# Kernel optimization log

Hardware: AMD Instinct MI355X
Metric: run time of the kernel (lower is better)

The kernel has to match this reference:

```python
import jax, jax.numpy as jnp
import numpy as np

B, H, W, C = 16, 112, 112, 128
WS, SS, NH = 7, 3, 4  # window_size, shift_size, num_heads
EPS = 1e-5


def _ln(x, g, b):
    m = jnp.mean(x, axis=-1, keepdims=True)
    v = jnp.var(x, axis=-1, keepdims=True)
    return (x - m) * jax.lax.rsqrt(v + EPS) * g + b


def _rel_index(w):
    # standard Swin relative-position index, [w*w, w*w] int
    coords = np.stack(np.meshgrid(np.arange(w), np.arange(w), indexing='ij'))  # [2,w,w]
    flat = coords.reshape(2, -1)                      # [2, N]
    rel = (flat[:, :, None] - flat[:, None, :]).transpose(1, 2, 0)  # [N,N,2]
    rel = rel + (w - 1)
    return rel[..., 0] * (2 * w - 1) + rel[..., 1]


def _attn_mask(Hp, Wp, w, s):
    # standard Swin shifted-window attention mask, [nW, N, N] float32 (0 / -100)
    img = np.zeros((Hp, Wp))
    cnt = 0
    for hs in (slice(0, -w), slice(-w, -s), slice(-s, None)):
        for ws_ in (slice(0, -w), slice(-w, -s), slice(-s, None)):
            img[hs, ws_] = cnt
            cnt += 1
    mw = img.reshape(Hp // w, w, Wp // w, w).transpose(0, 2, 1, 3).reshape(-1, w * w)
    d = mw[:, None, :] - mw[:, :, None]
    return np.where(d != 0, -100.0, 0.0).astype(np.float32)


def setup_inputs() -> dict:
    key = jax.random.key(0)
    ks = jax.random.split(key, 8)
    f = lambda k, shape: jax.random.normal(k, shape, dtype=jnp.float32) * 0.02
    return dict(
        x=jax.random.normal(ks[0], (B, H, W, C), dtype=jnp.float32),
        norm1_g=jnp.ones((C,), jnp.float32), norm1_b=jnp.zeros((C,), jnp.float32),
        qkv_w=f(ks[1], (C, 3 * C)), qkv_b=jnp.zeros((3 * C,), jnp.float32),
        rel_table=f(ks[2], ((2 * WS - 1) ** 2, NH)),
        proj_w=f(ks[3], (C, C)), proj_b=jnp.zeros((C,), jnp.float32),
        norm2_g=jnp.ones((C,), jnp.float32), norm2_b=jnp.zeros((C,), jnp.float32),
        fc1_w=f(ks[4], (C, 4 * C)), fc1_b=jnp.zeros((4 * C,), jnp.float32),
        fc2_w=f(ks[5], (4 * C, C)), fc2_b=jnp.zeros((C,), jnp.float32),
    )


def reference(x, norm1_g, norm1_b, qkv_w, qkv_b, rel_table, proj_w, proj_b,
              norm2_g, norm2_b, fc1_w, fc1_b, fc2_w, fc2_b):
    w, s, nH = WS, SS, NH
    hd = C // nH
    N = w * w
    scale = hd ** -0.5

    shortcut = x
    xn = _ln(x, norm1_g, norm1_b)
    # cyclic shift (H, W already multiples of w -> no padding)
    xs = jnp.roll(xn, (-s, -s), axis=(1, 2)) if s > 0 else xn
    # window partition -> [B*nW, N, C]
    wins = xs.reshape(B, H // w, w, W // w, w, C).transpose(0, 1, 3, 2, 4, 5).reshape(-1, N, C)

    qkv = wins @ qkv_w + qkv_b  # [M, N, 3C]
    q, k, v = [t.reshape(-1, N, nH, hd).transpose(0, 2, 1, 3)
               for t in jnp.split(qkv, 3, axis=-1)]
    attn = jnp.einsum('mhqd,mhkd->mhqk', q * scale, k)  # [M, nH, N, N]

    idx = _rel_index(w)  # static numpy [N, N]
    bias = rel_table[idx.reshape(-1)].reshape(N, N, nH).transpose(2, 0, 1)  # [nH, N, N]
    attn = attn + bias[None]

    if s > 0:
        mask = jnp.asarray(_attn_mask(H, W, w, s))  # [nW, N, N] static
        nW = mask.shape[0]
        attn = (attn.reshape(B, nW, nH, N, N) + mask[None, :, None]).reshape(-1, nH, N, N)

    attn = jax.nn.softmax(attn, axis=-1)
    out = jnp.einsum('mhqk,mhkd->mhqd', attn, v).transpose(0, 2, 1, 3).reshape(-1, N, C)
    out = out @ proj_w + proj_b

    # window reverse + unshift
    x_attn = out.reshape(B, H // w, W // w, w, w, C).transpose(0, 1, 3, 2, 4, 5).reshape(B, H, W, C)
    if s > 0:
        x_attn = jnp.roll(x_attn, (s, s), axis=(1, 2))

    x1 = shortcut + x_attn
    xn2 = _ln(x1, norm2_g, norm2_b)
    hdd = jax.nn.gelu(xn2 @ fc1_w + fc1_b, approximate=False)  # torch nn.GELU (exact)
    return x1 + (hdd @ fc2_w + fc2_b)
```

## Files before the change

kernel.cpp:

```cpp
#include <hip/hip_runtime.h>
#include <stdint.h>

typedef unsigned short u16;
typedef unsigned int   u32;
typedef __attribute__((ext_vector_type(8))) short bh8;
typedef __attribute__((ext_vector_type(4))) float f32x4;

#define SCALE 0.17677669529663687f
#define MFMA  __builtin_amdgcn_mfma_f32_16x16x32_bf16

#define WS_QKV  0
#define WS_PROJ 49152
#define WS_F1   65536
#define WS_F2   131072
#define WS_M    196608
#define WS_QB   327680

__device__ __forceinline__ u16 f2bf(float f){
    u32 i; __builtin_memcpy(&i,&f,4); i += 0x7fffu + ((i>>16)&1u); return (u16)(i>>16);
}
__device__ __forceinline__ u32 cvtpk(float lo, float hi){
    u32 r; asm("v_cvt_pk_bf16_f32 %0, %1, %2" : "=v"(r) : "v"(lo), "v"(hi)); return r;
}
__device__ __forceinline__ float rcpf(float v){
    float r; asm("v_rcp_f32 %0, %1" : "=v"(r) : "v"(v)); return r;
}
union BH8U { bh8 v; u32 u[4]; };

__global__ void prep_k(const float* __restrict__ qkvw, const float* __restrict__ projw,
                       const float* __restrict__ f1w,  const float* __restrict__ f2w,
                       const float* __restrict__ rel,  const float* __restrict__ qkvb,
                       u16* __restrict__ ws)
{
    int idx = blockIdx.x * 256 + threadIdx.x;
    if (idx < 49152) {
        int c = idx / 384, j = idx % 384;
        float v = qkvw[idx] * (j < 128 ? SCALE : 1.0f);
        ws[WS_QKV + j * 128 + c] = f2bf(v);
    } else if (idx < 65536) {
        int i = idx - 49152; int k = i >> 7, j = i & 127;
        int pk = (k & ~31) | ((k & 15) << 1) | ((k >> 4) & 1);
        ws[WS_PROJ + j * 128 + pk] = f2bf(projw[i]);
    } else if (idx < 131072) {
        int i = idx - 65536; int c = i >> 9, j = i & 511;
        ws[WS_F1 + j * 128 + c] = f2bf(f1w[i]);
    } else if (idx < 196608) {
        int i = idx - 131072; int k = i >> 7, j = i & 127;
        int pk = (k & ~31) | ((k & 15) << 1) | ((k >> 4) & 1);
        ws[WS_F2 + j * 512 + pk] = f2bf(f2w[i]);
    } else if (idx < 262144) {
        int m = idx - 196608;
        int jr = m & 3, lane = (m >> 2) & 63, tct = (m >> 8) & 15;
        int h = (m >> 12) & 3, cls = (m >> 14) & 3;
        int rt = tct >> 2, ct = tct & 3;
        int row = rt * 16 + (lane >> 4) * 4 + jr, key = ct * 16 + (lane & 15);
        float v;
        if (row < 49 && key < 49) {
            int ri = row / 7, rc = row % 7, ki = key / 7, kc = key % 7;
            v = rel[((ri - ki + 6) * 13 + (rc - kc + 6)) * 4 + h];
            int rH = (cls & 2) ? (ri < 4 ? 1 : 2) : 0, rW = (cls & 1) ? (rc < 4 ? 1 : 2) : 0;
            int kH = (cls & 2) ? (ki < 4 ? 1 : 2) : 0, kW = (cls & 1) ? (kc < 4 ? 1 : 2) : 0;
            if (rH * 3 + rW != kH * 3 + kW) v -= 100.0f;
        } else v = -30000.0f;
        ((float*)(ws + WS_M))[m] = v;
    } else if (idx < 262528) {
        int j = idx - 262144;
        ((float*)(ws + WS_QB))[j] = qkvb[j] * (j < 128 ? SCALE : 1.0f);
    }
}

__global__ __launch_bounds__(256, 3) void swin_attn_k(
    const float* __restrict__ x, const float* __restrict__ n1g, const float* __restrict__ n1b,
    const float* __restrict__ projb, const u16* __restrict__ ws, float* __restrict__ out)
{
    __shared__ u16 arena[16384];
    __shared__ u16 vt[9216];
    const int tid = threadIdx.x, h = tid >> 6, lane = tid & 63;
    const int c15 = lane & 15, g = lane >> 4;
    const int m = blockIdx.x, b = m >> 8, hb = (m >> 4) & 15, wb = m & 15;
    const int cls = ((hb == 15) ? 2 : 0) | ((wb == 15) ? 1 : 0);
    const float* QB = (const float*)(ws + WS_QB);
    const float* Mb = (const float*)(ws + WS_M) + (size_t)((cls * 4 + h) * 16) * 256;

    {
        const int t = h * 16 + (lane >> 2), ss = lane & 3;
        const int td = (t * 37) >> 8, tm = t - td * 7;
        int hs = hb * 7 + td + 3;  if (hs >= 112) hs -= 112;
        int wsw = wb * 7 + tm + 3; if (wsw >= 112) wsw -= 112;
        const float* px = x + (size_t)((b * 112 + hs) * 112 + wsw) * 128 + ss * 32;
        float4 xv[8];
        #pragma unroll
        for (int i = 0; i < 8; ++i) xv[i] = *(const float4*)(px + i * 4);
        float s = 0.f, q = 0.f;
        #pragma unroll
        for (int i = 0; i < 8; ++i) {
            s += xv[i].x + xv[i].y + xv[i].z + xv[i].w;
            q += xv[i].x*xv[i].x + xv[i].y*xv[i].y + xv[i].z*xv[i].z + xv[i].w*xv[i].w;
        }
        s += __shfl_xor(s, 1); q += __shfl_xor(q, 1);
        s += __shfl_xor(s, 2); q += __shfl_xor(q, 2);
        float mean = s * (1.f/128.f), var = q * (1.f/128.f) - mean * mean;
        float rstd = rsqrtf(var + 1e-5f);
        const float* pg = n1g + ss * 32; const float* pb = n1b + ss * 32;
        #pragma unroll
        for (int i = 0; i < 4; ++i) {
            float4 a = xv[2*i], c = xv[2*i+1];
            float4 g1 = *(const float4*)(pg + i*8),  g2 = *(const float4*)(pg + i*8 + 4);
            float4 b1 = *(const float4*)(pb + i*8),  b2 = *(const float4*)(pb + i*8 + 4);
            uint4 w;
            w.x = cvtpk((a.x-mean)*rstd*g1.x + b1.x, (a.y-mean)*rstd*g1.y + b1.y);
            w.y = cvtpk((a.z-mean)*rstd*g1.z + b1.z, (a.w-mean)*rstd*g1.w + b1.w);
            w.z = cvtpk((c.x-mean)*rstd*g2.x + b2.x, (c.y-mean)*rstd*g2.y + b2.y);
            w.w = cvtpk((c.z-mean)*rstd*g2.z + b2.z, (c.w-mean)*rstd*g2.w + b2.w);
            *(uint4*)&arena[t * 136 + ss * 32 + i * 8] = w;
        }
    }
    __syncthreads();

    {
        bh8 avf[2][4];
        #pragma unroll
        for (int jt = 0; jt < 2; ++jt)
            #pragma unroll
            for (int kc = 0; kc < 4; ++kc)
                avf[jt][kc] = *(const bh8*)&ws[WS_QKV + (256 + h*32 + jt*16 + c15)*128 + kc*32 + g*8];
        const float vb0 = QB[256 + h*32 + c15], vb1 = QB[256 + h*32 + 16 + c15];
        #pragma unroll
        for (int tt = 0; tt < 4; ++tt) {
            bh8 xf[4];
            #pragma unroll
            for (int kc = 0; kc < 4; ++kc)
                xf[kc] = *(const bh8*)&arena[(tt*16 + c15)*136 + kc*32 + g*8];
            f32x4 D0 = {0,0,0,0}, D1 = {0,0,0,0};
            #pragma unroll
            for (int kc = 0; kc < 4; ++kc) { D0 = MFMA(xf[kc], avf[0][kc], D0, 0,0,0); D1 = MFMA(xf[kc], avf[1][kc], D1, 0,0,0); }
            uint2 p0, p1;
            p0.x = cvtpk(D0[0]+vb0, D0[1]+vb0); p0.y = cvtpk(D0[2]+vb0, D0[3]+vb0);
            p1.x = cvtpk(D1[0]+vb1, D1[1]+vb1); p1.y = cvtpk(D1[2]+vb1, D1[3]+vb1);
            *(uint2*)&vt[h*2304 + c15*72        + tt*16 + g*4] = p0;
            *(uint2*)&vt[h*2304 + (16+c15)*72   + tt*16 + g*4] = p1;
        }
    }

    bh8 qf[4], kf[4];
    {
        bh8 aqf[2][4], akf[2][4];
        #pragma unroll
        for (int jt = 0; jt < 2; ++jt)
            #pragma unroll
            for (int kc = 0; kc < 4; ++kc) {
                aqf[jt][kc] = *(const bh8*)&ws[WS_QKV + (      h*32 + jt*16 + c15)*128 + kc*32 + g*8];
                akf[jt][kc] = *(const bh8*)&ws[WS_QKV + (128 + h*32 + jt*16 + c15)*128 + kc*32 + g*8];
            }
        const float4 qb0 = *(const float4*)(QB + h*32 + g*4);
        const float4 qb1 = *(const float4*)(QB + h*32 + 16 + g*4);
        const float4 kb0 = *(const float4*)(QB + 128 + h*32 + g*4);
        const float4 kb1 = *(const float4*)(QB + 128 + h*32 + 16 + g*4);
        #pragma unroll
        for (int tt = 0; tt < 4; ++tt) {
            bh8 xf[4];
            #pragma unroll
            for (int kc = 0; kc < 4; ++kc)
                xf[kc] = *(const bh8*)&arena[(tt*16 + c15)*136 + kc*32 + g*8];
            f32x4 Dq0={0,0,0,0}, Dq1={0,0,0,0}, Dk0={0,0,0,0}, Dk1={0,0,0,0};
            #pragma unroll
            for (int kc = 0; kc < 4; ++kc) {
                Dq0 = MFMA(aqf[0][kc], xf[kc], Dq0, 0,0,0);
                Dq1 = MFMA(aqf[1][kc], xf[kc], Dq1, 0,0,0);
                Dk0 = MFMA(akf[0][kc], xf[kc], Dk0, 0,0,0);
                Dk1 = MFMA(akf[1][kc], xf[kc], Dk1, 0,0,0);
            }
            BH8U qu, ku;
            qu.u[0] = cvtpk(Dq0[0]+qb0.x, Dq0[1]+qb0.y); qu.u[1] = cvtpk(Dq0[2]+qb0.z, Dq0[3]+qb0.w);
            qu.u[2] = cvtpk(Dq1[0]+qb1.x, Dq1[1]+qb1.y); qu.u[3] = cvtpk(Dq1[2]+qb1.z, Dq1[3]+qb1.w);
            ku.u[0] = cvtpk(Dk0[0]+kb0.x, Dk0[1]+kb0.y); ku.u[1] = cvtpk(Dk0[2]+kb0.z, Dk0[3]+kb0.w);
            ku.u[2] = cvtpk(Dk1[0]+kb1.x, Dk1[1]+kb1.y); ku.u[3] = cvtpk(Dk1[2]+kb1.z, Dk1[3]+kb1.w);
            qf[tt] = qu.v; kf[tt] = ku.v;
        }
    }
    __syncthreads();

    f32x4 p[4][4]; f32x4 inv4[4];
    #pragma unroll
    for (int rt = 0; rt < 4; ++rt) {
        #pragma unroll
        for (int ct = 0; ct < 4; ++ct) {
            f32x4 macc = *(const f32x4*)(Mb + (rt*4 + ct)*256 + lane*4);
            p[rt][ct] = MFMA(qf[rt], kf[ct], macc, 0,0,0);
        }
        #pragma unroll
        for (int ct = 0; ct < 4; ++ct)
            #pragma unroll
            for (int jr = 0; jr < 4; ++jr) p[rt][ct][jr] = __expf(p[rt][ct][jr]);
        f32x4 t = p[rt][0] + p[rt][1] + p[rt][2] + p[rt][3];
        #pragma unroll
        for (int jr = 0; jr < 4; ++jr) {
            float v = t[jr];
            v += __shfl_xor(v, 1); v += __shfl_xor(v, 2);
            v += __shfl_xor(v, 4); v += __shfl_xor(v, 8);
            inv4[rt][jr] = rcpf(v);
        }
    }

    char* Pbase = (char*)arena + h * 8192;
    #pragma unroll
    for (int rt = 0; rt < 4; ++rt)
        #pragma unroll
        for (int jr = 0; jr < 4; ++jr) {
            const int row = rt*16 + g*4 + jr, sw = (row & 7) << 4;
            #pragma unroll
            for (int ct = 0; ct < 4; ++ct)
                *(u16*)(Pbase + ((row*128 + (ct*16 + c15)*2) ^ sw)) = f2bf(p[rt][ct][jr]);
        }
    asm volatile("s_waitcnt lgkmcnt(0)" ::: "memory");

    f32x4 o[4][2];
    #pragma unroll
    for (int rt = 0; rt < 4; ++rt) { o[rt][0] = (f32x4){0,0,0,0}; o[rt][1] = (f32x4){0,0,0,0}; }
    {
        bh8 vf[2][2];
        #pragma unroll
        for (int ct = 0; ct < 2; ++ct)
            #pragma unroll
            for (int kc = 0; kc < 2; ++kc)
                vf[ct][kc] = *(const bh8*)&vt[h*2304 + (ct*16 + c15)*72 + kc*32 + g*8];
        #pragma unroll
        for (int rt = 0; rt < 4; ++rt) {
            const int row = rt*16 + c15, sw = (row & 7) << 4;
            #pragma unroll
            for (int kc = 0; kc < 2; ++kc) {
                bh8 pa = *(const bh8*)(Pbase + ((row*128 + kc*64 + g*16) ^ sw));
                o[rt][0] = MFMA(pa, vf[0][kc], o[rt][0], 0,0,0);
                o[rt][1] = MFMA(pa, vf[1][kc], o[rt][1], 0,0,0);
            }
        }
    }
    __syncthreads();

    #pragma unroll
    for (int rt = 0; rt < 4; ++rt)
        #pragma unroll
        for (int jr = 0; jr < 4; ++jr) {
            const int row = rt*16 + g*4 + jr;
            u32 pk_ = cvtpk(o[rt][0][jr] * inv4[rt][jr], o[rt][1][jr] * inv4[rt][jr]);
            *(u32*)&arena[row*136 + h*32 + 2*c15] = pk_;
        }
    __syncthreads();

    {
        bh8 wfp[2][4];
        #pragma unroll
        for (int ct2 = 0; ct2 < 2; ++ct2)
            #pragma unroll
            for (int kc = 0; kc < 4; ++kc)
                wfp[ct2][kc] = *(const bh8*)&ws[WS_PROJ + (h*32 + ct2*16 + c15)*128 + kc*32 + g*8];
        f32x4 pacc[4][2];
        #pragma unroll
        for (int rt = 0; rt < 4; ++rt) { pacc[rt][0] = (f32x4){0,0,0,0}; pacc[rt][1] = (f32x4){0,0,0,0}; }
        #pragma unroll
        for (int rt = 0; rt < 4; ++rt) {
            bh8 af[4];
            #pragma unroll
            for (int kc = 0; kc < 4; ++kc)
                af[kc] = *(const bh8*)&arena[(rt*16 + c15)*136 + kc*32 + g*8];
            #pragma unroll
            for (int kc = 0; kc < 4; ++kc) {
                pacc[rt][0] = MFMA(af[kc], wfp[0][kc], pacc[rt][0], 0,0,0);
                pacc[rt][1] = MFMA(af[kc], wfp[1][kc], pacc[rt][1], 0,0,0);
            }
        }
        const int col0 = h*32 + c15, col1 = col0 + 16;
        const float pb0 = projb[col0], pb1 = projb[col1];
        #pragma unroll
        for (int rt = 0; rt < 4; ++rt)
            #pragma unroll
            for (int jr = 0; jr < 4; ++jr) {
                const int t = rt*16 + g*4 + jr;
                if (t < 49) {
                    const int td = (t * 37) >> 8, tm = t - td * 7;
                    int hs = hb*7 + td + 3;  if (hs >= 112) hs -= 112;
                    int wsw = wb*7 + tm + 3; if (wsw >= 112) wsw -= 112;
                    const size_t base = (size_t)((b*112 + hs)*112 + wsw) * 128;
                    out[base + col0] = pacc[rt][0][jr] + pb0 + x[base + col0];
                    out[base + col1] = pacc[rt][1][jr] + pb1 + x[base + col1];
                }
            }
    }
}

__global__ __launch_bounds__(256, 4) void swin_mlp_k(
    float* __restrict__ xio, const float* __restrict__ n2g, const float* __restrict__ n2b,
    const float* __restrict__ f1b, const float* __restrict__ f2b, const u16* __restrict__ ws)
{
    __shared__ u16 xnb[64 * 136];
    __shared__ u16 hbuf[64 * 136];
    const int tid = threadIdx.x, w = tid >> 6, lane = tid & 63;
    const int c15 = lane & 15, g = lane >> 4;
    const size_t tok0 = (size_t)blockIdx.x * 64;

    {
        const int t = w * 16 + (lane >> 2), ss = lane & 3;
        const float* px = xio + (tok0 + t) * 128 + ss * 32;
        float4 xv[8];
        #pragma unroll
        for (int i = 0; i < 8; ++i) xv[i] = *(const float4*)(px + i * 4);
        float s = 0.f, q = 0.f;
        #pragma unroll
        for (int i = 0; i < 8; ++i) {
            s += xv[i].x + xv[i].y + xv[i].z + xv[i].w;
            q += xv[i].x*xv[i].x + xv[i].y*xv[i].y + xv[i].z*xv[i].z + xv[i].w*xv[i].w;
        }
        s += __shfl_xor(s, 1); q += __shfl_xor(q, 1);
        s += __shfl_xor(s, 2); q += __shfl_xor(q, 2);
        float mean = s * (1.f/128.f), var = q * (1.f/128.f) - mean * mean;
        float rstd = rsqrtf(var + 1e-5f);
        const float* pg = n2g + ss * 32; const float* pb = n2b + ss * 32;
        #pragma unroll
        for (int i = 0; i < 4; ++i) {
            float4 a = xv[2*i], c = xv[2*i+1];
            float4 g1 = *(const float4*)(pg + i*8),  g2 = *(const float4*)(pg + i*8 + 4);
            float4 b1 = *(const float4*)(pb + i*8),  b2 = *(const float4*)(pb + i*8 + 4);
            uint4 wv;
            wv.x = cvtpk((a.x-mean)*rstd*g1.x + b1.x, (a.y-mean)*rstd*g1.y + b1.y);
            wv.y = cvtpk((a.z-mean)*rstd*g1.z + b1.z, (a.w-mean)*rstd*g1.w + b1.w);
            wv.z = cvtpk((c.x-mean)*rstd*g2.x + b2.x, (c.y-mean)*rstd*g2.y + b2.y);
            wv.w = cvtpk((c.z-mean)*rstd*g2.z + b2.z, (c.w-mean)*rstd*g2.w + b2.w);
            *(uint4*)&xnb[t * 136 + ss * 32 + i * 8] = wv;
        }
    }
    __syncthreads();

    f32x4 acc[4][2];
    #pragma unroll
    for (int rt = 0; rt < 4; ++rt) { acc[rt][0] = (f32x4){0,0,0,0}; acc[rt][1] = (f32x4){0,0,0,0}; }

    for (int chunk = 0; chunk < 4; ++chunk) {
        bh8 wf[2][4];
        #pragma unroll
        for (int jt = 0; jt < 2; ++jt)
            #pragma unroll
            for (int kc = 0; kc < 4; ++kc)
                wf[jt][kc] = *(const bh8*)&ws[WS_F1 + (chunk*128 + w*32 + jt*16 + c15)*128 + kc*32 + g*8];
        const float b1s0 = f1b[chunk*128 + w*32 + c15];
        const float b1s1 = f1b[chunk*128 + w*32 + 16 + c15];
        if (chunk) __syncthreads();
        #pragma unroll
        for (int rt = 0; rt < 4; ++rt) {
            bh8 af[4];
            #pragma unroll
            for (int kc = 0; kc < 4; ++kc)
                af[kc] = *(const bh8*)&xnb[(rt*16 + c15)*136 + kc*32 + g*8];
            f32x4 D0 = {0,0,0,0}, D1 = {0,0,0,0};
            #pragma unroll
            for (int kc = 0; kc < 4; ++kc) { D0 = MFMA(af[kc], wf[0][kc], D0, 0,0,0); D1 = MFMA(af[kc], wf[1][kc], D1, 0,0,0); }
            #pragma unroll
            for (int jr = 0; jr < 4; ++jr) {
                float h0 = D0[jr] + b1s0, h1 = D1[jr] + b1s1;
                h0 = 0.5f * h0 * (1.0f + erff(h0 * 0.70710678118654752f));
                h1 = 0.5f * h1 * (1.0f + erff(h1 * 0.70710678118654752f));
                *(u32*)&hbuf[(rt*16 + g*4 + jr)*136 + w*32 + 2*c15] = cvtpk(h0, h1);
            }
        }
        __syncthreads();
        bh8 wf2[2][4];
        #pragma unroll
        for (int ct2 = 0; ct2 < 2; ++ct2)
            #pragma unroll
            for (int kc = 0; kc < 4; ++kc)
                wf2[ct2][kc] = *(const bh8*)&ws[WS_F2 + (w*32 + ct2*16 + c15)*512 + chunk*128 + kc*32 + g*8];
        #pragma unroll
        for (int rt = 0; rt < 4; ++rt) {
            bh8 ha[4];
            #pragma unroll
            for (int kc = 0; kc < 4; ++kc)
                ha[kc] = *(const bh8*)&hbuf[(rt*16 + c15)*136 + kc*32 + g*8];
            #pragma unroll
            for (int kc = 0; kc < 4; ++kc) {
                acc[rt][0] = MFMA(ha[kc], wf2[0][kc], acc[rt][0], 0,0,0);
                acc[rt][1] = MFMA(ha[kc], wf2[1][kc], acc[rt][1], 0,0,0);
            }
        }
    }

    const int col0 = w*32 + c15, col1 = col0 + 16;
    const float cb0 = f2b[col0], cb1 = f2b[col1];
    #pragma unroll
    for (int rt = 0; rt < 4; ++rt)
        #pragma unroll
        for (int jr = 0; jr < 4; ++jr) {
            const size_t r = (tok0 + rt*16 + g*4 + jr) * 128;
            xio[r + col0] += acc[rt][0][jr] + cb0;
            xio[r + col1] += acc[rt][1][jr] + cb1;
        }
}

extern "C" void kernel_launch(void* const* d_in, const int* in_sizes, int n_in,
                              void* d_out, int out_size, void* d_ws, size_t ws_size,
                              hipStream_t stream)
{
    const float* x    = (const float*)d_in[0];
    const float* n1g  = (const float*)d_in[1];
    const float* n1b  = (const float*)d_in[2];
    const float* qkvw = (const float*)d_in[3];
    const float* qkvb = (const float*)d_in[4];
    const float* rel  = (const float*)d_in[5];
    const float* pw   = (const float*)d_in[6];
    const float* pb   = (const float*)d_in[7];
    const float* n2g  = (const float*)d_in[8];
    const float* n2b  = (const float*)d_in[9];
    const float* f1w  = (const float*)d_in[10];
    const float* f1b  = (const float*)d_in[11];
    const float* f2w  = (const float*)d_in[12];
    const float* f2b  = (const float*)d_in[13];
    float* out = (float*)d_out;
    u16* ws = (u16*)d_ws;

    prep_k<<<1026, 256, 0, stream>>>(qkvw, pw, f1w, f2w, rel, qkvb, ws);
    swin_attn_k<<<4096, 256, 0, stream>>>(x, n1g, n1b, pb, ws, out);
    swin_mlp_k<<<3136, 256, 0, stream>>>(out, n2g, n2b, f1b, f2b, ws);
}
```

Baseline: 288.3 us.

## Fuse MLP block into windowed attention kernel and use polynomial erf GELU

Merges the separate MLP kernel into the attention kernel, so each window block computes the residual, LayerNorm2, fc1+GELU and fc2 on its 49 tokens from shared memory. This removes the global write and re-read of the intermediate x1 tensor and one kernel launch. It also replaces erff with an Abramowitz-Stegun polynomial GELU, zero-pads the unused token rows, and XOR-swizzles the LDS layout for the MLP operands. The trade-offs: MLP work is padded from 49 to 64 rows per block, LayerNorm2 statistics come from bf16-rounded x1, and register pressure in the single kernel rises.

Result: slower. 332.6 us (+15.4%).

```diff
diff --git a/kernel.cpp b/kernel.cpp
--- a/kernel.cpp
+++ b/kernel.cpp
@@ -19,11 +19,27 @@
 __device__ __forceinline__ u16 f2bf(float f){
     u32 i; __builtin_memcpy(&i,&f,4); i += 0x7fffu + ((i>>16)&1u); return (u16)(i>>16);
 }
+__device__ __forceinline__ float bflo(u32 u){
+    u32 i = u << 16; float f; __builtin_memcpy(&f,&i,4); return f;
+}
+__device__ __forceinline__ float bfhi(u32 u){
+    u32 i = u & 0xffff0000u; float f; __builtin_memcpy(&f,&i,4); return f;
+}
 __device__ __forceinline__ u32 cvtpk(float lo, float hi){
     u32 r; asm("v_cvt_pk_bf16_f32 %0, %1, %2" : "=v"(r) : "v"(lo), "v"(hi)); return r;
 }
 __device__ __forceinline__ float rcpf(float v){
     float r; asm("v_rcp_f32 %0, %1" : "=v"(r) : "v"(v)); return r;
+}
+__device__ __forceinline__ float gelu_f(float x){
+    float ax = fabsf(x);
+    float z  = ax * 0.70710678118654752f;
+    float t  = rcpf(fmaf(0.3275911f, z, 1.0f));
+    float p  = t * fmaf(t, fmaf(t, fmaf(t, fmaf(t, 1.061405429f, -1.453152027f),
+                                        1.421413741f), -0.284496736f), 0.254829592f);
+    float e  = __expf(-z * z);
+    float y  = fmaf(-p, e, 1.0f);
+    return fmaf(0.5f * ax, y, 0.5f * x);
 }
 union BH8U { bh8 v; u32 u[4]; };
 
@@ -69,12 +85,16 @@
     }
 }
 
-__global__ __launch_bounds__(256, 3) void swin_attn_k(
+__global__ __launch_bounds__(256, 3) void swin_fused_k(
     const float* __restrict__ x, const float* __restrict__ n1g, const float* __restrict__ n1b,
-    const float* __restrict__ projb, const u16* __restrict__ ws, float* __restrict__ out)
+    const float* __restrict__ projb, const float* __restrict__ n2g, const float* __restrict__ n2b,
+    const float* __restrict__ f1b, const float* __restrict__ f2b,
+    const u16* __restrict__ ws, float* __restrict__ out)
 {
     __shared__ u16 arena[16384];
-    __shared__ u16 vt[9216];
+    __shared__ u16 vtx[9216];
+    float* stats = (float*)&vtx[8704];
+
     const int tid = threadIdx.x, h = tid >> 6, lane = tid & 63;
     const int c15 = lane & 15, g = lane >> 4;
     const int m = blockIdx.x, b = m >> 8, hb = (m >> 4) & 15, wb = m & 15;
@@ -84,35 +104,40 @@
 
     {
         const int t = h * 16 + (lane >> 2), ss = lane & 3;
-        const int td = (t * 37) >> 8, tm = t - td * 7;
-        int hs = hb * 7 + td + 3;  if (hs >= 112) hs -= 112;
-        int wsw = wb * 7 + tm + 3; if (wsw >= 112) wsw -= 112;
-        const float* px = x + (size_t)((b * 112 + hs) * 112 + wsw) * 128 + ss * 32;
-        float4 xv[8];
-        #pragma unroll
-        for (int i = 0; i < 8; ++i) xv[i] = *(const float4*)(px + i * 4);
-        float s = 0.f, q = 0.f;
-        #pragma unroll
-        for (int i = 0; i < 8; ++i) {
-            s += xv[i].x + xv[i].y + xv[i].z + xv[i].w;
-            q += xv[i].x*xv[i].x + xv[i].y*xv[i].y + xv[i].z*xv[i].z + xv[i].w*xv[i].w;
-        }
-        s += __shfl_xor(s, 1); q += __shfl_xor(q, 1);
-        s += __shfl_xor(s, 2); q += __shfl_xor(q, 2);
-        float mean = s * (1.f/128.f), var = q * (1.f/128.f) - mean * mean;
-        float rstd = rsqrtf(var + 1e-5f);
-        const float* pg = n1g + ss * 32; const float* pb = n1b + ss * 32;
-        #pragma unroll
-        for (int i = 0; i < 4; ++i) {
-            float4 a = xv[2*i], c = xv[2*i+1];
-            float4 g1 = *(const float4*)(pg + i*8),  g2 = *(const float4*)(pg + i*8 + 4);
-            float4 b1 = *(const float4*)(pb + i*8),  b2 = *(const float4*)(pb + i*8 + 4);
-            uint4 w;
-            w.x = cvtpk((a.x-mean)*rstd*g1.x + b1.x, (a.y-mean)*rstd*g1.y + b1.y);
-            w.y = cvtpk((a.z-mean)*rstd*g1.z + b1.z, (a.w-mean)*rstd*g1.w + b1.w);
-            w.z = cvtpk((c.x-mean)*rstd*g2.x + b2.x, (c.y-mean)*rstd*g2.y + b2.y);
-            w.w = cvtpk((c.z-mean)*rstd*g2.z + b2.z, (c.w-mean)*rstd*g2.w + b2.w);
-            *(uint4*)&arena[t * 136 + ss * 32 + i * 8] = w;
+        if (t < 49) {
+            const int td = (t * 37) >> 8, tm = t - td * 7;
+            int hs = hb * 7 + td + 3;  if (hs >= 112) hs -= 112;
+            int wsw = wb * 7 + tm + 3; if (wsw >= 112) wsw -= 112;
+            const float* px = x + (size_t)((b * 112 + hs) * 112 + wsw) * 128 + ss * 32;
+            float4 xv[8];
+            #pragma unroll
+            for (int i = 0; i < 8; ++i) xv[i] = *(const float4*)(px + i * 4);
+            float s = 0.f, q = 0.f;
+            #pragma unroll
+            for (int i = 0; i < 8; ++i) {
+                s += xv[i].x + xv[i].y + xv[i].z + xv[i].w;
+                q += xv[i].x*xv[i].x + xv[i].y*xv[i].y + xv[i].z*xv[i].z + xv[i].w*xv[i].w;
+            }
+            s += __shfl_xor(s, 1); q += __shfl_xor(q, 1);
+            s += __shfl_xor(s, 2); q += __shfl_xor(q, 2);
+            float mean = s * (1.f/128.f), var = q * (1.f/128.f) - mean * mean;
+            float rstd = rsqrtf(var + 1e-5f);
+            const float* pg = n1g + ss * 32; const float* pb = n1b + ss * 32;
+            #pragma unroll
+            for (int i = 0; i < 4; ++i) {
+                float4 a = xv[2*i], c = xv[2*i+1];
+                float4 g1 = *(const float4*)(pg + i*8),  g2 = *(const float4*)(pg + i*8 + 4);
+                float4 b1 = *(const float4*)(pb + i*8),  b2 = *(const float4*)(pb + i*8 + 4);
+                uint4 w;
+                w.x = cvtpk((a.x-mean)*rstd*g1.x + b1.x, (a.y-mean)*rstd*g1.y + b1.y);
+                w.y = cvtpk((a.z-mean)*rstd*g1.z + b1.z, (a.w-mean)*rstd*g1.w + b1.w);
+                w.z = cvtpk((c.x-mean)*rstd*g2.x + b2.x, (c.y-mean)*rstd*g2.y + b2.y);
+                w.w = cvtpk((c.z-mean)*rstd*g2.z + b2.z, (c.w-mean)*rstd*g2.w + b2.w);
+                *(uint4*)&arena[t * 136 + ss * 32 + i * 8] = w;
+            }
+        } else {
+            #pragma unroll
+            for (int i = 0; i < 4; ++i) *(uint4*)&arena[t * 136 + (lane & 3) * 32 + i * 8] = (uint4){0,0,0,0};
         }
     }
     __syncthreads();
@@ -137,8 +162,8 @@
             uint2 p0, p1;
             p0.x = cvtpk(D0[0]+vb0, D0[1]+vb0); p0.y = cvtpk(D0[2]+vb0, D0[3]+vb0);
             p1.x = cvtpk(D1[0]+vb1, D1[1]+vb1); p1.y = cvtpk(D1[2]+vb1, D1[3]+vb1);
-            *(uint2*)&vt[h*2304 + c15*72        + tt*16 + g*4] = p0;
-            *(uint2*)&vt[h*2304 + (16+c15)*72   + tt*16 + g*4] = p1;
+            *(uint2*)&vtx[h*2304 + c15*72        + tt*16 + g*4] = p0;
+            *(uint2*)&vtx[h*2304 + (16+c15)*72   + tt*16 + g*4] = p1;
         }
     }
 
@@ -198,7 +223,7 @@
             float v = t[jr];
             v += __shfl_xor(v, 1); v += __shfl_xor(v, 2);
             v += __shfl_xor(v, 4); v += __shfl_xor(v, 8);
-            inv4[rt][jr] = rcpf(v);
+            inv4[rt][jr] = rcpf(v + 1e-30f);
         }
     }
 
@@ -223,7 +248,7 @@
         for (int ct = 0; ct < 2; ++ct)
             #pragma unroll
             for (int kc = 0; kc < 2; ++kc)
-                vf[ct][kc] = *(const bh8*)&vt[h*2304 + (ct*16 + c15)*72 + kc*32 + g*8];
+                vf[ct][kc] = *(const bh8*)&vtx[h*2304 + (ct*16 + c15)*72 + kc*32 + g*8];
         #pragma unroll
         for (int rt = 0; rt < 4; ++rt) {
             const int row = rt*16 + c15, sw = (row & 7) << 4;
@@ -247,6 +272,8 @@
         }
     __syncthreads();
 
+    const int col0 = h*32 + c15, col1 = col0 + 16;
+    float x1a[4][4], x1b[4][4];
     {
         bh8 wfp[2][4];
         #pragma unroll
@@ -269,8 +296,124 @@
                 pacc[rt][1] = MFMA(af[kc], wfp[1][kc], pacc[rt][1], 0,0,0);
             }
         }
-        const int col0 = h*32 + c15, col1 = col0 + 16;
         const float pb0 = projb[col0], pb1 = projb[col1];
+        #pragma unroll
+        for (int rt = 0; rt < 4; ++rt)
+            #pragma unroll
+            for (int jr = 0; jr < 4; ++jr) {
+                const int t = rt*16 + g*4 + jr;
+                float xr0 = 0.f, xr1 = 0.f;
+                if (t < 49) {
+                    const int td = (t * 37) >> 8, tm = t - td * 7;
+                    int hs = hb*7 + td + 3;  if (hs >= 112) hs -= 112;
+                    int wsw = wb*7 + tm + 3; if (wsw >= 112) wsw -= 112;
+                    const size_t base = (size_t)((b*112 + hs)*112 + wsw) * 128;
+                    xr0 = x[base + col0]; xr1 = x[base + col1];
+                }
+                x1a[rt][jr] = pacc[rt][0][jr] + pb0 + xr0;
+                x1b[rt][jr] = pacc[rt][1][jr] + pb1 + xr1;
+                vtx[t*136 + col0] = f2bf(x1a[rt][jr]);
+                vtx[t*136 + col1] = f2bf(x1b[rt][jr]);
+            }
+    }
+    __syncthreads();
+
+    {
+        const int t = h * 16 + (lane >> 2), ss = lane & 3;
+        const u16* pr = &vtx[t*136 + ss*32];
+        float s = 0.f, q = 0.f;
+        #pragma unroll
+        for (int i = 0; i < 4; ++i) {
+            uint4 v = *(const uint4*)(pr + i*8);
+            float e0=bflo(v.x), e1=bfhi(v.x), e2=bflo(v.y), e3=bfhi(v.y);
+            float e4=bflo(v.z), e5=bfhi(v.z), e6=bflo(v.w), e7=bfhi(v.w);
+            s += e0+e1+e2+e3+e4+e5+e6+e7;
+            q += e0*e0+e1*e1+e2*e2+e3*e3+e4*e4+e5*e5+e6*e6+e7*e7;
+        }
+        s += __shfl_xor(s, 1); q += __shfl_xor(q, 1);
+        s += __shfl_xor(s, 2); q += __shfl_xor(q, 2);
+        float mean = s * (1.f/128.f), var = q * (1.f/128.f) - mean * mean;
+        float rstd = rsqrtf(var + 1e-5f);
+        if (ss == 0) { stats[t*2] = mean; stats[t*2+1] = rstd; }
+    }
+    __syncthreads();
+
+    char* XN = (char*)arena;
+    char* HB = (char*)arena + 16384;
+    #pragma unroll
+    for (int rt = 0; rt < 4; ++rt) {
+        const int row = rt*16 + c15;
+        const float mean = stats[row*2], rstd = stats[row*2+1];
+        #pragma unroll
+        for (int kc = 0; kc < 4; ++kc) {
+            BH8U xu; xu.v = *(const bh8*)&vtx[row*136 + kc*32 + g*8];
+            const float* pg = n2g + kc*32 + g*8; const float* pb = n2b + kc*32 + g*8;
+            float4 g1 = *(const float4*)pg, g2 = *(const float4*)(pg + 4);
+            float4 b1 = *(const float4*)pb, b2 = *(const float4*)(pb + 4);
+            BH8U w;
+            w.u[0] = cvtpk((bflo(xu.u[0])-mean)*rstd*g1.x + b1.x, (bfhi(xu.u[0])-mean)*rstd*g1.y + b1.y);
+            w.u[1] = cvtpk((bflo(xu.u[1])-mean)*rstd*g1.z + b1.z, (bfhi(xu.u[1])-mean)*rstd*g1.w + b1.w);
+            w.u[2] = cvtpk((bflo(xu.u[2])-mean)*rstd*g2.x + b2.x, (bfhi(xu.u[2])-mean)*rstd*g2.y + b2.y);
+            w.u[3] = cvtpk((bflo(xu.u[3])-mean)*rstd*g2.z + b2.z, (bfhi(xu.u[3])-mean)*rstd*g2.w + b2.w);
+            *(bh8*)(XN + ((row*256 + kc*64 + g*16) ^ ((row & 7) << 4))) = w.v;
+        }
+    }
+    __syncthreads();
+
+    f32x4 acc[4][2];
+    #pragma unroll
+    for (int rt = 0; rt < 4; ++rt) { acc[rt][0] = (f32x4){0,0,0,0}; acc[rt][1] = (f32x4){0,0,0,0}; }
+    for (int chunk = 0; chunk < 4; ++chunk) {
+        bh8 wf1[2][4];
+        #pragma unroll
+        for (int jt = 0; jt < 2; ++jt)
+            #pragma unroll
+            for (int kc = 0; kc < 4; ++kc)
+                wf1[jt][kc] = *(const bh8*)&ws[WS_F1 + (chunk*128 + h*32 + jt*16 + c15)*128 + kc*32 + g*8];
+        const float b1s0 = f1b[chunk*128 + h*32 + c15];
+        const float b1s1 = f1b[chunk*128 + h*32 + 16 + c15];
+        #pragma unroll
+        for (int rt = 0; rt < 4; ++rt) {
+            const int arow = rt*16 + c15;
+            bh8 af[4];
+            #pragma unroll
+            for (int kc = 0; kc < 4; ++kc)
+                af[kc] = *(const bh8*)(XN + ((arow*256 + kc*64 + g*16) ^ ((arow & 7) << 4)));
+            f32x4 D0 = {0,0,0,0}, D1 = {0,0,0,0};
+            #pragma unroll
+            for (int kc = 0; kc < 4; ++kc) { D0 = MFMA(af[kc], wf1[0][kc], D0, 0,0,0); D1 = MFMA(af[kc], wf1[1][kc], D1, 0,0,0); }
+            #pragma unroll
+            for (int jr = 0; jr < 4; ++jr) {
+                const int row = rt*16 + g*4 + jr;
+                u32 hp = cvtpk(gelu_f(D0[jr] + b1s0), gelu_f(D1[jr] + b1s1));
+                *(u32*)(HB + ((row*256 + h*64 + c15*4) ^ ((row & 7) << 4))) = hp;
+            }
+        }
+        __syncthreads();
+        bh8 wf2[2][4];
+        #pragma unroll
+        for (int ct2 = 0; ct2 < 2; ++ct2)
+            #pragma unroll
+            for (int kc = 0; kc < 4; ++kc)
+                wf2[ct2][kc] = *(const bh8*)&ws[WS_F2 + (h*32 + ct2*16 + c15)*512 + chunk*128 + kc*32 + g*8];
+        #pragma unroll
+        for (int rt = 0; rt < 4; ++rt) {
+            const int arow = rt*16 + c15;
+            bh8 ha[4];
+            #pragma unroll
+            for (int kc = 0; kc < 4; ++kc)
+                ha[kc] = *(const bh8*)(HB + ((arow*256 + kc*64 + g*16) ^ ((arow & 7) << 4)));
+            #pragma unroll
+            for (int kc = 0; kc < 4; ++kc) {
+                acc[rt][0] = MFMA(ha[kc], wf2[0][kc], acc[rt][0], 0,0,0);
+                acc[rt][1] = MFMA(ha[kc], wf2[1][kc], acc[rt][1], 0,0,0);
+            }
+        }
+        __syncthreads();
+    }
+
+    {
+        const float cb0 = f2b[col0], cb1 = f2b[col1];
         #pragma unroll
         for (int rt = 0; rt < 4; ++rt)
             #pragma unroll
@@ -281,117 +424,11 @@
                     int hs = hb*7 + td + 3;  if (hs >= 112) hs -= 112;
                     int wsw = wb*7 + tm + 3; if (wsw >= 112) wsw -= 112;
                     const size_t base = (size_t)((b*112 + hs)*112 + wsw) * 128;
-                    out[base + col0] = pacc[rt][0][jr] + pb0 + x[base + col0];
-                    out[base + col1] = pacc[rt][1][jr] + pb1 + x[base + col1];
+                    out[base + col0] = x1a[rt][jr] + acc[rt][0][jr] + cb0;
+                    out[base + col1] = x1b[rt][jr] + acc[rt][1][jr] + cb1;
                 }
             }
     }
-}
-
-__global__ __launch_bounds__(256, 4) void swin_mlp_k(
-    float* __restrict__ xio, const float* __restrict__ n2g, const float* __restrict__ n2b,
-    const float* __restrict__ f1b, const float* __restrict__ f2b, const u16* __restrict__ ws)
-{
-    __shared__ u16 xnb[64 * 136];
-    __shared__ u16 hbuf[64 * 136];
-    const int tid = threadIdx.x, w = tid >> 6, lane = tid & 63;
-    const int c15 = lane & 15, g = lane >> 4;
-    const size_t tok0 = (size_t)blockIdx.x * 64;
-
-    {
-        const int t = w * 16 + (lane >> 2), ss = lane & 3;
-        const float* px = xio + (tok0 + t) * 128 + ss * 32;
-        float4 xv[8];
-        #pragma unroll
-        for (int i = 0; i < 8; ++i) xv[i] = *(const float4*)(px + i * 4);
-        float s = 0.f, q = 0.f;
-        #pragma unroll
-        for (int i = 0; i < 8; ++i) {
-            s += xv[i].x + xv[i].y + xv[i].z + xv[i].w;
-            q += xv[i].x*xv[i].x + xv[i].y*xv[i].y + xv[i].z*xv[i].z + xv[i].w*xv[i].w;
-        }
-        s += __shfl_xor(s, 1); q += __shfl_xor(q, 1);
-        s += __shfl_xor(s, 2); q += __shfl_xor(q, 2);
-        float mean = s * (1.f/128.f), var = q * (1.f/128.f) - mean * mean;
-        float rstd = rsqrtf(var + 1e-5f);
-        const float* pg = n2g + ss * 32; const float* pb = n2b + ss * 32;
-        #pragma unroll
-        for (int i = 0; i < 4; ++i) {
-            float4 a = xv[2*i], c = xv[2*i+1];
-            float4 g1 = *(const float4*)(pg + i*8),  g2 = *(const float4*)(pg + i*8 + 4);
-            float4 b1 = *(const float4*)(pb + i*8),  b2 = *(const float4*)(pb + i*8 + 4);
-            uint4 wv;
-            wv.x = cvtpk((a.x-mean)*rstd*g1.x + b1.x, (a.y-mean)*rstd*g1.y + b1.y);
-            wv.y = cvtpk((a.z-mean)*rstd*g1.z + b1.z, (a.w-mean)*rstd*g1.w + b1.w);
-            wv.z = cvtpk((c.x-mean)*rstd*g2.x + b2.x, (c.y-mean)*rstd*g2.y + b2.y);
-            wv.w = cvtpk((c.z-mean)*rstd*g2.z + b2.z, (c.w-mean)*rstd*g2.w + b2.w);
-            *(uint4*)&xnb[t * 136 + ss * 32 + i * 8] = wv;
-        }
-    }
-    __syncthreads();
-
-    f32x4 acc[4][2];
-    #pragma unroll
-    for (int rt = 0; rt < 4; ++rt) { acc[rt][0] = (f32x4){0,0,0,0}; acc[rt][1] = (f32x4){0,0,0,0}; }
-
-    for (int chunk = 0; chunk < 4; ++chunk) {
-        bh8 wf[2][4];
-        #pragma unroll
-        for (int jt = 0; jt < 2; ++jt)
-            #pragma unroll
-            for (int kc = 0; kc < 4; ++kc)
-                wf[jt][kc] = *(const bh8*)&ws[WS_F1 + (chunk*128 + w*32 + jt*16 + c15)*128 + kc*32 + g*8];
-        const float b1s0 = f1b[chunk*128 + w*32 + c15];
-        const float b1s1 = f1b[chunk*128 + w*32 + 16 + c15];
-        if (chunk) __syncthreads();
-        #pragma unroll
-        for (int rt = 0; rt < 4; ++rt) {
-            bh8 af[4];
-            #pragma unroll
-            for (int kc = 0; kc < 4; ++kc)
-                af[kc] = *(const bh8*)&xnb[(rt*16 + c15)*136 + kc*32 + g*8];
-            f32x4 D0 = {0,0,0,0}, D1 = {0,0,0,0};
-            #pragma unroll
-            for (int kc = 0; kc < 4; ++kc) { D0 = MFMA(af[kc], wf[0][kc], D0, 0,0,0); D1 = MFMA(af[kc], wf[1][kc], D1, 0,0,0); }
-            #pragma unroll
-            for (int jr = 0; jr < 4; ++jr) {
-                float h0 = D0[jr] + b1s0, h1 = D1[jr] + b1s1;
-                h0 = 0.5f * h0 * (1.0f + erff(h0 * 0.70710678118654752f));
-                h1 = 0.5f * h1 * (1.0f + erff(h1 * 0.70710678118654752f));
-                *(u32*)&hbuf[(rt*16 + g*4 + jr)*136 + w*32 + 2*c15] = cvtpk(h0, h1);
-            }
-        }
-        __syncthreads();
-        bh8 wf2[2][4];
-        #pragma unroll
-        for (int ct2 = 0; ct2 < 2; ++ct2)
-            #pragma unroll
-            for (int kc = 0; kc < 4; ++kc)
-                wf2[ct2][kc] = *(const bh8*)&ws[WS_F2 + (w*32 + ct2*16 + c15)*512 + chunk*128 + kc*32 + g*8];
-        #pragma unroll
-        for (int rt = 0; rt < 4; ++rt) {
-            bh8 ha[4];
-            #pragma unroll
-            for (int kc = 0; kc < 4; ++kc)
-                ha[kc] = *(const bh8*)&hbuf[(rt*16 + c15)*136 + kc*32 + g*8];
-            #pragma unroll
-            for (int kc = 0; kc < 4; ++kc) {
-                acc[rt][0] = MFMA(ha[kc], wf2[0][kc], acc[rt][0], 0,0,0);
-                acc[rt][1] = MFMA(ha[kc], wf2[1][kc], acc[rt][1], 0,0,0);
-            }
-        }
-    }
-
-    const int col0 = w*32 + c15, col1 = col0 + 16;
-    const float cb0 = f2b[col0], cb1 = f2b[col1];
-    #pragma unroll
-    for (int rt = 0; rt < 4; ++rt)
-        #pragma unroll
-        for (int jr = 0; jr < 4; ++jr) {
-            const size_t r = (tok0 + rt*16 + g*4 + jr) * 128;
-            xio[r + col0] += acc[rt][0][jr] + cb0;
-            xio[r + col1] += acc[rt][1][jr] + cb1;
-        }
 }
 
 extern "C" void kernel_launch(void* const* d_in, const int* in_sizes, int n_in,
@@ -416,6 +453,5 @@
     u16* ws = (u16*)d_ws;
 
     prep_k<<<1026, 256, 0, stream>>>(qkvw, pw, f1w, f2w, rel, qkvb, ws);
-    swin_attn_k<<<4096, 256, 0, stream>>>(x, n1g, n1b, pb, ws, out);
-    swin_mlp_k<<<3136, 256, 0, stream>>>(out, n2g, n2b, f1b, f2b, ws);
-}
+    swin_fused_k<<<4096, 256, 0, stream>>>(x, n1g, n1b, pb, n2g, n2b, f1b, f2b, ws, out);
+}
```

## Fold LayerNorm2 affine into fc1 weights and use polynomial GELU approximation

Applied to the files above, without the earlier changes.

The norm2 gamma is folded into the fc1 weights, and gamma/beta projections are precomputed into per-output scale and offset vectors. The MLP kernel therefore stages raw x in bf16 and applies mean/rstd after the MFMA using per-row stats kept in shared memory. The exact erff-based GELU is replaced with an Abramowitz-Stegun polynomial using rcp and exp, cutting the VALU cost of the epilogue. The attention kernel also skips global loads for padded token rows (zeroing them instead) and guards the softmax reciprocal. The risks are precision loss from converting un-normalized x to bf16 and the approximation error of the GELU polynomial.

New measurement: 274.5 us. 1.05x faster.

```diff
diff --git a/kernel.cpp b/kernel.cpp
--- a/kernel.cpp
+++ b/kernel.cpp
@@ -15,22 +15,41 @@
 #define WS_F2   131072
 #define WS_M    196608
 #define WS_QB   327680
+#define WS_S1   328448
+#define WS_T1   329472
 
 __device__ __forceinline__ u16 f2bf(float f){
     u32 i; __builtin_memcpy(&i,&f,4); i += 0x7fffu + ((i>>16)&1u); return (u16)(i>>16);
 }
+__device__ __forceinline__ float bflo(u32 u){
+    u32 i = u << 16; float f; __builtin_memcpy(&f,&i,4); return f;
+}
+__device__ __forceinline__ float bfhi(u32 u){
+    u32 i = u & 0xffff0000u; float f; __builtin_memcpy(&f,&i,4); return f;
+}
 __device__ __forceinline__ u32 cvtpk(float lo, float hi){
     u32 r; asm("v_cvt_pk_bf16_f32 %0, %1, %2" : "=v"(r) : "v"(lo), "v"(hi)); return r;
 }
 __device__ __forceinline__ float rcpf(float v){
     float r; asm("v_rcp_f32 %0, %1" : "=v"(r) : "v"(v)); return r;
+}
+__device__ __forceinline__ float gelu_f(float x){
+    float ax = fabsf(x);
+    float z  = ax * 0.70710678118654752f;
+    float t  = rcpf(fmaf(0.3275911f, z, 1.0f));
+    float p  = t * fmaf(t, fmaf(t, fmaf(t, fmaf(t, 1.061405429f, -1.453152027f),
+                                        1.421413741f), -0.284496736f), 0.254829592f);
+    float e  = __expf(-z * z);
+    float y  = fmaf(-p, e, 1.0f);
+    return fmaf(0.5f * ax, y, 0.5f * x);
 }
 union BH8U { bh8 v; u32 u[4]; };
 
 __global__ void prep_k(const float* __restrict__ qkvw, const float* __restrict__ projw,
                        const float* __restrict__ f1w,  const float* __restrict__ f2w,
                        const float* __restrict__ rel,  const float* __restrict__ qkvb,
-                       u16* __restrict__ ws)
+                       const float* __restrict__ n2g,  const float* __restrict__ n2b,
+                       const float* __restrict__ f1b,  u16* __restrict__ ws)
 {
     int idx = blockIdx.x * 256 + threadIdx.x;
     if (idx < 49152) {
@@ -43,7 +62,7 @@
         ws[WS_PROJ + j * 128 + pk] = f2bf(projw[i]);
     } else if (idx < 131072) {
         int i = idx - 65536; int c = i >> 9, j = i & 511;
-        ws[WS_F1 + j * 128 + c] = f2bf(f1w[i]);
+        ws[WS_F1 + j * 128 + c] = f2bf(f1w[i] * n2g[c]);
     } else if (idx < 196608) {
         int i = idx - 131072; int k = i >> 7, j = i & 127;
         int pk = (k & ~31) | ((k & 15) << 1) | ((k >> 4) & 1);
@@ -66,6 +85,16 @@
     } else if (idx < 262528) {
         int j = idx - 262144;
         ((float*)(ws + WS_QB))[j] = qkvb[j] * (j < 128 ? SCALE : 1.0f);
+    } else if (idx < 263040) {
+        int j = idx - 262528;
+        float s1 = 0.f, t1 = 0.f;
+        for (int c = 0; c < 128; ++c) {
+            float w = f1w[c * 512 + j];
+            s1 = fmaf(n2g[c], w, s1);
+            t1 = fmaf(n2b[c], w, t1);
+        }
+        ((float*)(ws + WS_S1))[j] = s1;
+        ((float*)(ws + WS_T1))[j] = f1b[j] + t1;
     }
 }
 
@@ -84,35 +113,40 @@
 
     {
         const int t = h * 16 + (lane >> 2), ss = lane & 3;
-        const int td = (t * 37) >> 8, tm = t - td * 7;
-        int hs = hb * 7 + td + 3;  if (hs >= 112) hs -= 112;
-        int wsw = wb * 7 + tm + 3; if (wsw >= 112) wsw -= 112;
-        const float* px = x + (size_t)((b * 112 + hs) * 112 + wsw) * 128 + ss * 32;
-        float4 xv[8];
-        #pragma unroll
-        for (int i = 0; i < 8; ++i) xv[i] = *(const float4*)(px + i * 4);
-        float s = 0.f, q = 0.f;
-        #pragma unroll
-        for (int i = 0; i < 8; ++i) {
-            s += xv[i].x + xv[i].y + xv[i].z + xv[i].w;
-            q += xv[i].x*xv[i].x + xv[i].y*xv[i].y + xv[i].z*xv[i].z + xv[i].w*xv[i].w;
-        }
-        s += __shfl_xor(s, 1); q += __shfl_xor(q, 1);
-        s += __shfl_xor(s, 2); q += __shfl_xor(q, 2);
-        float mean = s * (1.f/128.f), var = q * (1.f/128.f) - mean * mean;
-        float rstd = rsqrtf(var + 1e-5f);
-        const float* pg = n1g + ss * 32; const float* pb = n1b + ss * 32;
-        #pragma unroll
-        for (int i = 0; i < 4; ++i) {
-            float4 a = xv[2*i], c = xv[2*i+1];
-            float4 g1 = *(const float4*)(pg + i*8),  g2 = *(const float4*)(pg + i*8 + 4);
-            float4 b1 = *(const float4*)(pb + i*8),  b2 = *(const float4*)(pb + i*8 + 4);
-            uint4 w;
-            w.x = cvtpk((a.x-mean)*rstd*g1.x + b1.x, (a.y-mean)*rstd*g1.y + b1.y);
-            w.y = cvtpk((a.z-mean)*rstd*g1.z + b1.z, (a.w-mean)*rstd*g1.w + b1.w);
-            w.z = cvtpk((c.x-mean)*rstd*g2.x + b2.x, (c.y-mean)*rstd*g2.y + b2.y);
-            w.w = cvtpk((c.z-mean)*rstd*g2.z + b2.z, (c.w-mean)*rstd*g2.w + b2.w);
-            *(uint4*)&arena[t * 136 + ss * 32 + i * 8] = w;
+        if (t < 49) {
+            const int td = (t * 37) >> 8, tm = t - td * 7;
+            int hs = hb * 7 + td + 3;  if (hs >= 112) hs -= 112;
+            int wsw = wb * 7 + tm + 3; if (wsw >= 112) wsw -= 112;
+            const float* px = x + (size_t)((b * 112 + hs) * 112 + wsw) * 128 + ss * 32;
+            float4 xv[8];
+            #pragma unroll
+            for (int i = 0; i < 8; ++i) xv[i] = *(const float4*)(px + i * 4);
+            float s = 0.f, q = 0.f;
+            #pragma unroll
+            for (int i = 0; i < 8; ++i) {
+                s += xv[i].x + xv[i].y + xv[i].z + xv[i].w;
+                q += xv[i].x*xv[i].x + xv[i].y*xv[i].y + xv[i].z*xv[i].z + xv[i].w*xv[i].w;
+            }
+            s += __shfl_xor(s, 1); q += __shfl_xor(q, 1);
+            s += __shfl_xor(s, 2); q += __shfl_xor(q, 2);
+            float mean = s * (1.f/128.f), var = q * (1.f/128.f) - mean * mean;
+            float rstd = rsqrtf(var + 1e-5f);
+            const float* pg = n1g + ss * 32; const float* pb = n1b + ss * 32;
+            #pragma unroll
+            for (int i = 0; i < 4; ++i) {
+                float4 a = xv[2*i], c = xv[2*i+1];
+                float4 g1 = *(const float4*)(pg + i*8),  g2 = *(const float4*)(pg + i*8 + 4);
+                float4 b1 = *(const float4*)(pb + i*8),  b2 = *(const float4*)(pb + i*8 + 4);
+                uint4 w;
+                w.x = cvtpk((a.x-mean)*rstd*g1.x + b1.x, (a.y-mean)*rstd*g1.y + b1.y);
+                w.y = cvtpk((a.z-mean)*rstd*g1.z + b1.z, (a.w-mean)*rstd*g1.w + b1.w);
+                w.z = cvtpk((c.x-mean)*rstd*g2.x + b2.x, (c.y-mean)*rstd*g2.y + b2.y);
+                w.w = cvtpk((c.z-mean)*rstd*g2.z + b2.z, (c.w-mean)*rstd*g2.w + b2.w);
+                *(uint4*)&arena[t * 136 + ss * 32 + i * 8] = w;
+            }
+        } else {
+            #pragma unroll
+            for (int i = 0; i < 4; ++i) *(uint4*)&arena[t * 136 + (lane & 3) * 32 + i * 8] = (uint4){0,0,0,0};
         }
     }
     __syncthreads();
@@ -198,7 +232,7 @@
             float v = t[jr];
             v += __shfl_xor(v, 1); v += __shfl_xor(v, 2);
             v += __shfl_xor(v, 4); v += __shfl_xor(v, 8);
-            inv4[rt][jr] = rcpf(v);
+            inv4[rt][jr] = rcpf(v + 1e-30f);
         }
     }
 
@@ -289,14 +323,16 @@
 }
 
 __global__ __launch_bounds__(256, 4) void swin_mlp_k(
-    float* __restrict__ xio, const float* __restrict__ n2g, const float* __restrict__ n2b,
-    const float* __restrict__ f1b, const float* __restrict__ f2b, const u16* __restrict__ ws)
+    float* __restrict__ xio, const float* __restrict__ f2b, const u16* __restrict__ ws)
 {
     __shared__ u16 xnb[64 * 136];
     __shared__ u16 hbuf[64 * 136];
+    __shared__ float2 stats[64];
     const int tid = threadIdx.x, w = tid >> 6, lane = tid & 63;
     const int c15 = lane & 15, g = lane >> 4;
     const size_t tok0 = (size_t)blockIdx.x * 64;
+    const float* S1 = (const float*)(ws + WS_S1);
+    const float* T1 = (const float*)(ws + WS_T1);
 
     {
         const int t = w * 16 + (lane >> 2), ss = lane & 3;
@@ -314,19 +350,15 @@
         s += __shfl_xor(s, 2); q += __shfl_xor(q, 2);
         float mean = s * (1.f/128.f), var = q * (1.f/128.f) - mean * mean;
         float rstd = rsqrtf(var + 1e-5f);
-        const float* pg = n2g + ss * 32; const float* pb = n2b + ss * 32;
         #pragma unroll
         for (int i = 0; i < 4; ++i) {
             float4 a = xv[2*i], c = xv[2*i+1];
-            float4 g1 = *(const float4*)(pg + i*8),  g2 = *(const float4*)(pg + i*8 + 4);
-            float4 b1 = *(const float4*)(pb + i*8),  b2 = *(const float4*)(pb + i*8 + 4);
             uint4 wv;
-            wv.x = cvtpk((a.x-mean)*rstd*g1.x + b1.x, (a.y-mean)*rstd*g1.y + b1.y);
-            wv.y = cvtpk((a.z-mean)*rstd*g1.z + b1.z, (a.w-mean)*rstd*g1.w + b1.w);
-            wv.z = cvtpk((c.x-mean)*rstd*g2.x + b2.x, (c.y-mean)*rstd*g2.y + b2.y);
-            wv.w = cvtpk((c.z-mean)*rstd*g2.z + b2.z, (c.w-mean)*rstd*g2.w + b2.w);
+            wv.x = cvtpk(a.x, a.y); wv.y = cvtpk(a.z, a.w);
+            wv.z = cvtpk(c.x, c.y); wv.w = cvtpk(c.z, c.w);
             *(uint4*)&xnb[t * 136 + ss * 32 + i * 8] = wv;
         }
+        if (ss == 0) stats[t] = (float2){rstd, rstd * mean};
     }
     __syncthreads();
 
@@ -334,15 +366,17 @@
     #pragma unroll
     for (int rt = 0; rt < 4; ++rt) { acc[rt][0] = (f32x4){0,0,0,0}; acc[rt][1] = (f32x4){0,0,0,0}; }
 
+    #pragma unroll
     for (int chunk = 0; chunk < 4; ++chunk) {
-        bh8 wf[2][4];
+        bh8 wf1[2][4];
         #pragma unroll
         for (int jt = 0; jt < 2; ++jt)
             #pragma unroll
             for (int kc = 0; kc < 4; ++kc)
-                wf[jt][kc] = *(const bh8*)&ws[WS_F1 + (chunk*128 + w*32 + jt*16 + c15)*128 + kc*32 + g*8];
-        const float b1s0 = f1b[chunk*128 + w*32 + c15];
-        const float b1s1 = f1b[chunk*128 + w*32 + 16 + c15];
+                wf1[jt][kc] = *(const bh8*)&ws[WS_F1 + (chunk*128 + w*32 + jt*16 + c15)*128 + kc*32 + g*8];
+        const int j0 = chunk*128 + w*32 + c15;
+        const float s1a = S1[j0], s1b = S1[j0 + 16];
+        const float t1a = T1[j0], t1b = T1[j0 + 16];
         if (chunk) __syncthreads();
         #pragma unroll
         for (int rt = 0; rt < 4; ++rt) {
@@ -352,13 +386,14 @@
                 af[kc] = *(const bh8*)&xnb[(rt*16 + c15)*136 + kc*32 + g*8];
             f32x4 D0 = {0,0,0,0}, D1 = {0,0,0,0};
             #pragma unroll
-            for (int kc = 0; kc < 4; ++kc) { D0 = MFMA(af[kc], wf[0][kc], D0, 0,0,0); D1 = MFMA(af[kc], wf[1][kc], D1, 0,0,0); }
+            for (int kc = 0; kc < 4; ++kc) { D0 = MFMA(af[kc], wf1[0][kc], D0, 0,0,0); D1 = MFMA(af[kc], wf1[1][kc], D1, 0,0,0); }
             #pragma unroll
             for (int jr = 0; jr < 4; ++jr) {
-                float h0 = D0[jr] + b1s0, h1 = D1[jr] + b1s1;
-                h0 = 0.5f * h0 * (1.0f + erff(h0 * 0.70710678118654752f));
-                h1 = 0.5f * h1 * (1.0f + erff(h1 * 0.70710678118654752f));
-                *(u32*)&hbuf[(rt*16 + g*4 + jr)*136 + w*32 + 2*c15] = cvtpk(h0, h1);
+                const int row = rt*16 + g*4 + jr;
+                float2 st = stats[row];
+                float h0 = gelu_f(fmaf(st.x, D0[jr], fmaf(-st.y, s1a, t1a)));
+                float h1 = gelu_f(fmaf(st.x, D1[jr], fmaf(-st.y, s1b, t1b)));
+                *(u32*)&hbuf[row*136 + w*32 + 2*c15] = cvtpk(h0, h1);
             }
         }
         __syncthreads();
@@ -415,7 +450,7 @@
     float* out = (float*)d_out;
     u16* ws = (u16*)d_ws;
 
-    prep_k<<<1026, 256, 0, stream>>>(qkvw, pw, f1w, f2w, rel, qkvb, ws);
+    prep_k<<<1028, 256, 0, stream>>>(qkvw, pw, f1w, f2w, rel, qkvb, n2g, n2b, f1b, ws);
     swin_attn_k<<<4096, 256, 0, stream>>>(x, n1g, n1b, pb, ws, out);
-    swin_mlp_k<<<3136, 256, 0, stream>>>(out, n2g, n2b, f1b, f2b, ws);
-}
+    swin_mlp_k<<<3136, 256, 0, stream>>>(out, f2b, ws);
+}
```
